# Performance work log

Measured on AMD Instinct MI355X. Metric: run time of the kernel, lower is better.

The kernel has to match this reference:

```python
import jax, jax.numpy as jnp
import numpy as np

N_NODES = 50000
N_EDGES = 800000
D = 128


def gcn_conv(x, W, b, src, dst, num_nodes):
    """PyG GCNConv: x @ W, add self-loops, symmetric normalization, scatter-add, + bias."""
    x = x @ W  # [N, out]
    loop = jnp.arange(num_nodes, dtype=src.dtype)
    s = jnp.concatenate([src, loop])  # [E+N]
    d = jnp.concatenate([dst, loop])
    w = jnp.ones(s.shape[0], x.dtype)  # edge_weight=None -> ones (self-loop fill=1)
    deg = jax.ops.segment_sum(w, d, num_segments=num_nodes)  # [N]
    dinv = jnp.where(deg > 0, jax.lax.rsqrt(deg), 0.0)
    norm = dinv[s] * dinv[d]  # [E+N]
    out = jax.ops.segment_sum(x[s] * norm[:, None], d, num_segments=num_nodes)
    return out + b


def setup_inputs() -> dict:
    key = jax.random.key(0)
    ks = jax.random.split(key, 8)
    sc = 1.0 / np.sqrt(D)
    x = jax.random.normal(ks[0], (N_NODES, D), dtype=jnp.float32)
    edge_index = jax.random.randint(ks[1], (2, N_EDGES), 0, N_NODES)
    W1 = jax.random.normal(ks[2], (D, D), dtype=jnp.float32) * sc
    W2 = jax.random.normal(ks[3], (D, D), dtype=jnp.float32) * sc
    W3 = jax.random.normal(ks[4], (D, D), dtype=jnp.float32) * sc
    b1 = jnp.zeros((D,), jnp.float32)
    b2 = jnp.zeros((D,), jnp.float32)
    b3 = jnp.zeros((D,), jnp.float32)
    return {"x": x, "edge_index": edge_index, "W1": W1, "b1": b1,
            "W2": W2, "b2": b2, "W3": W3, "b3": b3}


def reference(x, edge_index, W1, b1, W2, b2, W3, b3):
    src, dst = edge_index[0], edge_index[1]
    n = x.shape[0]
    x = jax.nn.relu(gcn_conv(x, W1, b1, src, dst, n))
    x = jax.nn.relu(gcn_conv(x, W2, b2, src, dst, n))
    return gcn_conv(x, W3, b3, src, dst, n)
```

## Files before the change

kernel.cpp:

```cpp
#include <hip/hip_runtime.h>
#include <hip/hip_fp16.h>
#include <math.h>

#define D 128
#define PADH 136

typedef __attribute__((ext_vector_type(8))) _Float16 half8;
typedef __attribute__((ext_vector_type(4))) float f32x4;


__global__ void prep_kernel(const float* __restrict__ W1, const float* __restrict__ W2,
                            const float* __restrict__ W3, __half* __restrict__ WhT,
                            int* __restrict__ cnt, int N) {
    int i = blockIdx.x * blockDim.x + threadIdx.x;
    if (i < 3 * D * D) {
        int l = i >> 14;
        int j = i & 16383;
        int n = j >> 7, k = j & 127;
        const float* W = (l == 0) ? W1 : (l == 1) ? W2 : W3;
        WhT[(size_t)i] = __float2half(W[(size_t)k * D + n]);
    }
    if (i < N) cnt[i] = 0;
}


__global__ void count_rank_kernel(const int* __restrict__ dst, int* __restrict__ cnt,
                                  int* __restrict__ rank, int E) {
    int e0 = (blockIdx.x * blockDim.x + threadIdx.x) * 8;
    if (e0 + 7 < E) {
        int4 da = *(const int4*)(dst + e0);
        int4 db = *(const int4*)(dst + e0 + 4);
        int4 ra, rb;
        ra.x = atomicAdd(&cnt[da.x], 1);
        ra.y = atomicAdd(&cnt[da.y], 1);
        ra.z = atomicAdd(&cnt[da.z], 1);
        ra.w = atomicAdd(&cnt[da.w], 1);
        rb.x = atomicAdd(&cnt[db.x], 1);
        rb.y = atomicAdd(&cnt[db.y], 1);
        rb.z = atomicAdd(&cnt[db.z], 1);
        rb.w = atomicAdd(&cnt[db.w], 1);
        *(int4*)(rank + e0)     = ra;
        *(int4*)(rank + e0 + 4) = rb;
    } else {
        for (int e = e0; e < E; ++e) rank[e] = atomicAdd(&cnt[dst[e]], 1);
    }
}

__global__ __launch_bounds__(1024) void scan_kernel(const int* __restrict__ cnt,
                                                    int* __restrict__ rowptr,
                                                    float* __restrict__ dinv,
                                                    int N) {
    __shared__ int wsum[16];
    int tid  = threadIdx.x;
    int lane = tid & 63;
    int wid  = tid >> 6;
    int C = ((N + 4095) / 4096) * 4;
    int start = tid * C;
    int end   = start + C; if (end > N) end = N;

    int local = 0;
    int i = start;
    for (; i + 3 < end; i += 4) {
        int4 v = *(const int4*)(cnt + i);
        local += v.x + v.y + v.z + v.w;
    }
    for (; i < end; ++i) local += cnt[i];

    int sc = local;
    #pragma unroll
    for (int off = 1; off < 64; off <<= 1) {
        int t = __shfl_up(sc, off, 64);
        if (lane >= off) sc += t;
    }
    if (lane == 63) wsum[wid] = sc;
    __syncthreads();
    if (tid < 16) {
        int w = wsum[tid];
        #pragma unroll
        for (int off = 1; off < 16; off <<= 1) {
            int t = __shfl_up(w, off, 16);
            if (tid >= off) w += t;
        }
        wsum[tid] = w;
    }
    __syncthreads();
    int run = ((wid > 0) ? wsum[wid - 1] : 0) + (sc - local);

    i = start;
    for (; i + 3 < end; i += 4) {
        int4 v = *(const int4*)(cnt + i);
        int4 rp;
        rp.x = run;
        rp.y = rp.x + v.x;
        rp.z = rp.y + v.y;
        rp.w = rp.z + v.z;
        run  = rp.w + v.w;
        *(int4*)(rowptr + i) = rp;
        float4 dv;
        dv.x = rsqrtf((float)v.x + 1.0f);
        dv.y = rsqrtf((float)v.y + 1.0f);
        dv.z = rsqrtf((float)v.z + 1.0f);
        dv.w = rsqrtf((float)v.w + 1.0f);
        *(float4*)(dinv + i) = dv;
    }
    for (; i < end; ++i) {
        int v = cnt[i];
        rowptr[i] = run; run += v;
        dinv[i] = rsqrtf((float)v + 1.0f);
    }
    if (tid == 0) rowptr[N] = wsum[15];
}


#define GATHER(vv, cc) __half2 vv = ((const __half2*)(g + (size_t)(cc) * D))[lane]

__device__ __forceinline__ float2 gather_row(const __half* __restrict__ g,
                                             const int* __restrict__ rowptr,
                                             const int* __restrict__ col,
                                             int row, int lane) {
    int s = rowptr[row], e = rowptr[row + 1];
    __half2 hself = ((const __half2*)(g + (size_t)row * D))[lane];
    float2 a0 = __half22float2(hself);
    float2 a1 = make_float2(0.f, 0.f), a2 = make_float2(0.f, 0.f),
           a3 = make_float2(0.f, 0.f), a4 = make_float2(0.f, 0.f),
           a5 = make_float2(0.f, 0.f), a6 = make_float2(0.f, 0.f),
           a7 = make_float2(0.f, 0.f);

    for (int base = s; base < e; base += 64) {
        int idx = base + lane;
        int myc = (idx < e) ? col[idx] : 0;
        int nb  = min(64, e - base);
        int j = 0;
        for (; j + 16 <= nb; j += 16) {
            int c0 = __shfl(myc, j + 0),  c1 = __shfl(myc, j + 1);
            int c2 = __shfl(myc, j + 2),  c3 = __shfl(myc, j + 3);
            int c4 = __shfl(myc, j + 4),  c5 = __shfl(myc, j + 5);
            int c6 = __shfl(myc, j + 6),  c7 = __shfl(myc, j + 7);
            int c8 = __shfl(myc, j + 8),  c9 = __shfl(myc, j + 9);
            int cA = __shfl(myc, j + 10), cB = __shfl(myc, j + 11);
            int cC = __shfl(myc, j + 12), cD = __shfl(myc, j + 13);
            int cE = __shfl(myc, j + 14), cF = __shfl(myc, j + 15);
            GATHER(v0, c0); GATHER(v1, c1); GATHER(v2, c2); GATHER(v3, c3);
            GATHER(v4, c4); GATHER(v5, c5); GATHER(v6, c6); GATHER(v7, c7);
            GATHER(v8, c8); GATHER(v9, c9); GATHER(vA, cA); GATHER(vB, cB);
            GATHER(vC, cC); GATHER(vD, cD); GATHER(vE, cE); GATHER(vF, cF);
            a0.x += __low2float(v0); a0.y += __high2float(v0);
            a1.x += __low2float(v1); a1.y += __high2float(v1);
            a2.x += __low2float(v2); a2.y += __high2float(v2);
            a3.x += __low2float(v3); a3.y += __high2float(v3);
            a4.x += __low2float(v4); a4.y += __high2float(v4);
            a5.x += __low2float(v5); a5.y += __high2float(v5);
            a6.x += __low2float(v6); a6.y += __high2float(v6);
            a7.x += __low2float(v7); a7.y += __high2float(v7);
            a0.x += __low2float(v8); a0.y += __high2float(v8);
            a1.x += __low2float(v9); a1.y += __high2float(v9);
            a2.x += __low2float(vA); a2.y += __high2float(vA);
            a3.x += __low2float(vB); a3.y += __high2float(vB);
            a4.x += __low2float(vC); a4.y += __high2float(vC);
            a5.x += __low2float(vD); a5.y += __high2float(vD);
            a6.x += __low2float(vE); a6.y += __high2float(vE);
            a7.x += __low2float(vF); a7.y += __high2float(vF);
        }
        for (; j + 8 <= nb; j += 8) {
            int c0 = __shfl(myc, j + 0), c1 = __shfl(myc, j + 1);
            int c2 = __shfl(myc, j + 2), c3 = __shfl(myc, j + 3);
            int c4 = __shfl(myc, j + 4), c5 = __shfl(myc, j + 5);
            int c6 = __shfl(myc, j + 6), c7 = __shfl(myc, j + 7);
            GATHER(v0, c0); GATHER(v1, c1); GATHER(v2, c2); GATHER(v3, c3);
            GATHER(v4, c4); GATHER(v5, c5); GATHER(v6, c6); GATHER(v7, c7);
            a0.x += __low2float(v0); a0.y += __high2float(v0);
            a1.x += __low2float(v1); a1.y += __high2float(v1);
            a2.x += __low2float(v2); a2.y += __high2float(v2);
            a3.x += __low2float(v3); a3.y += __high2float(v3);
            a4.x += __low2float(v4); a4.y += __high2float(v4);
            a5.x += __low2float(v5); a5.y += __high2float(v5);
            a6.x += __low2float(v6); a6.y += __high2float(v6);
            a7.x += __low2float(v7); a7.y += __high2float(v7);
        }
        for (; j + 4 <= nb; j += 4) {
            int c0 = __shfl(myc, j + 0), c1 = __shfl(myc, j + 1);
            int c2 = __shfl(myc, j + 2), c3 = __shfl(myc, j + 3);
            GATHER(v0, c0); GATHER(v1, c1); GATHER(v2, c2); GATHER(v3, c3);
            a0.x += __low2float(v0); a0.y += __high2float(v0);
            a1.x += __low2float(v1); a1.y += __high2float(v1);
            a2.x += __low2float(v2); a2.y += __high2float(v2);
            a3.x += __low2float(v3); a3.y += __high2float(v3);
        }
        for (; j < nb; ++j) {
            int c = __shfl(myc, j);
            GATHER(v, c);
            a0.x += __low2float(v); a0.y += __high2float(v);
        }
    }
    a0.x += a1.x + a2.x + a3.x + a4.x + a5.x + a6.x + a7.x;
    a0.y += a1.y + a2.y + a3.y + a4.y + a5.y + a6.y + a7.y;
    return a0;
}


__global__ __launch_bounds__(256) void fill_gemm1_kernel(
    const int* __restrict__ src, const int* __restrict__ dst,
    const int* __restrict__ rank, const int* __restrict__ rowptr,
    int* __restrict__ col, int E, int fill_blocks,
    const float* __restrict__ X, const __half* __restrict__ WhT,
    const float* __restrict__ dinv, __half* __restrict__ Y, int M) {
    int tid = threadIdx.x;
    if ((int)blockIdx.x < fill_blocks) {
        int e0 = (blockIdx.x * 256 + tid) * 8;
        if (e0 + 7 < E) {
            int4 da = *(const int4*)(dst + e0);
            int4 db = *(const int4*)(dst + e0 + 4);
            int4 ra = *(const int4*)(rank + e0);
            int4 rb = *(const int4*)(rank + e0 + 4);
            int4 sa = *(const int4*)(src + e0);
            int4 sb = *(const int4*)(src + e0 + 4);
            int p0 = rowptr[da.x] + ra.x;
            int p1 = rowptr[da.y] + ra.y;
            int p2 = rowptr[da.z] + ra.z;
            int p3 = rowptr[da.w] + ra.w;
            int p4 = rowptr[db.x] + rb.x;
            int p5 = rowptr[db.y] + rb.y;
            int p6 = rowptr[db.z] + rb.z;
            int p7 = rowptr[db.w] + rb.w;
            col[p0] = sa.x; col[p1] = sa.y; col[p2] = sa.z; col[p3] = sa.w;
            col[p4] = sb.x; col[p5] = sb.y; col[p6] = sb.z; col[p7] = sb.w;
        } else {
            for (int e = e0; e < E; ++e) col[rowptr[dst[e]] + rank[e]] = src[e];
        }
        return;
    }
    int bid  = blockIdx.x - fill_blocks;
    int wave = tid >> 6;
    int lane = tid & 63;
    int quad = lane >> 4;
    int l16  = lane & 15;
    int m0   = bid * 64 + wave * 16;
    if (m0 >= M) return;

    f32x4 acc[8];
    #pragma unroll
    for (int t = 0; t < 8; ++t) acc[t] = (f32x4)0.0f;

    const float* xrow = X + (size_t)(m0 + l16) * D;

    #pragma unroll
    for (int ks = 0; ks < 4; ++ks) {
        int k0 = ks * 32 + quad * 8;
        float4 x0 = *(const float4*)(xrow + k0);
        float4 x1 = *(const float4*)(xrow + k0 + 4);
        half8 a;
        a[0] = (_Float16)x0.x; a[1] = (_Float16)x0.y;
        a[2] = (_Float16)x0.z; a[3] = (_Float16)x0.w;
        a[4] = (_Float16)x1.x; a[5] = (_Float16)x1.y;
        a[6] = (_Float16)x1.z; a[7] = (_Float16)x1.w;
        #pragma unroll
        for (int t = 0; t < 8; ++t) {
            half8 b = *(const half8*)(WhT + (size_t)(t * 16 + l16) * D + k0);
            acc[t] = __builtin_amdgcn_mfma_f32_16x16x32_f16(a, b, acc[t], 0, 0, 0);
        }
    }

    float4 dv = *(const float4*)(dinv + m0 + quad * 4);
    float dvs[4] = {dv.x, dv.y, dv.z, dv.w};
    #pragma unroll
    for (int t = 0; t < 8; ++t) {
        #pragma unroll
        for (int r = 0; r < 4; ++r) {
            int grow = m0 + quad * 4 + r;
            Y[(size_t)grow * D + t * 16 + l16] = __float2half(acc[t][r] * dvs[r]);
        }
    }
}


__global__ __launch_bounds__(256) void agg_gemm_kernel(
    const __half* __restrict__ ysIn, const int* __restrict__ rowptr,
    const int* __restrict__ col, const float* __restrict__ dinv,
    const float* __restrict__ bias, const __half* __restrict__ WhT,
    __half* __restrict__ ysOut, int M) {
    __shared__ __half lds_h[16 * PADH];
    int tid  = threadIdx.x;
    int wave = tid >> 6;
    int lane = tid & 63;
    int rbase = blockIdx.x * 16;

    float2 bb = ((const float2*)bias)[lane];
    #pragma unroll
    for (int t = 0; t < 4; ++t) {
        int row = rbase + wave * 4 + t;
        if (row < M) {
            float2 a = gather_row(ysIn, rowptr, col, row, lane);
            float dv = dinv[row];
            float rx = bb.x + dv * a.x;
            float ry = bb.y + dv * a.y;
            __half2 hv = __floats2half2_rn(fmaxf(rx, 0.f), fmaxf(ry, 0.f));
            ((__half2*)(lds_h + (size_t)(wave * 4 + t) * PADH))[lane] = hv;
        }
    }
    __syncthreads();

    if (rbase >= M) return;
    int quad = lane >> 4;
    int l16  = lane & 15;
    int t0   = wave * 2;

    f32x4 acc0 = (f32x4)0.0f, acc1 = (f32x4)0.0f;
    const __half* arow = lds_h + (size_t)l16 * PADH;

    #pragma unroll
    for (int ks = 0; ks < 4; ++ks) {
        int k0 = ks * 32 + quad * 8;
        half8 a  = *(const half8*)(arow + k0);
        half8 b0 = *(const half8*)(WhT + (size_t)((t0 + 0) * 16 + l16) * D + k0);
        half8 b1 = *(const half8*)(WhT + (size_t)((t0 + 1) * 16 + l16) * D + k0);
        acc0 = __builtin_amdgcn_mfma_f32_16x16x32_f16(a, b0, acc0, 0, 0, 0);
        acc1 = __builtin_amdgcn_mfma_f32_16x16x32_f16(a, b1, acc1, 0, 0, 0);
    }

    #pragma unroll
    for (int r = 0; r < 4; ++r) {
        int grow = rbase + quad * 4 + r;
        if (grow < M) {
            float dvr = dinv[grow];
            ysOut[(size_t)grow * D + (t0 + 0) * 16 + l16] = __float2half(acc0[r] * dvr);
            ysOut[(size_t)grow * D + (t0 + 1) * 16 + l16] = __float2half(acc1[r] * dvr);
        }
    }
}


__global__ __launch_bounds__(256) void agg_final_kernel(
    const __half* __restrict__ ys, const int* __restrict__ rowptr,
    const int* __restrict__ col, const float* __restrict__ dinv,
    const float* __restrict__ b, float* __restrict__ out, int N) {
    int gwave = (blockIdx.x * blockDim.x + threadIdx.x) >> 6;
    int lane  = threadIdx.x & 63;
    if (gwave >= N) return;
    float2 a  = gather_row(ys, rowptr, col, gwave, lane);
    float dv  = dinv[gwave];
    float2 bb = ((const float2*)b)[lane];
    ((float2*)(out + (size_t)gwave * D))[lane] = make_float2(bb.x + dv * a.x, bb.y + dv * a.y);
}


extern "C" void kernel_launch(void* const* d_in, const int* in_sizes, int n_in,
                              void* d_out, int out_size, void* d_ws, size_t ws_size,
                              hipStream_t stream) {
    const float* x   = (const float*)d_in[0];
    const int*   ei  = (const int*)d_in[1];
    const float* W1  = (const float*)d_in[2];
    const float* b1  = (const float*)d_in[3];
    const float* W2  = (const float*)d_in[4];
    const float* b2  = (const float*)d_in[5];
    const float* W3  = (const float*)d_in[6];
    const float* b3  = (const float*)d_in[7];
    float* out = (float*)d_out;

    const int N = in_sizes[0] / D;
    const int E = in_sizes[1] / 2;
    const int* src = ei;
    const int* dst = ei + E;

    char* ws = (char*)d_ws;
    size_t off = 0;
    auto alloc = [&](size_t bytes) {
        void* p = ws + off;
        off = (off + bytes + 255) & ~(size_t)255;
        return p;
    };
    __half* ys    = (__half*)alloc((size_t)N * D * sizeof(__half));
    __half* hs    = (__half*)alloc((size_t)N * D * sizeof(__half));
    int*   cnt    = (int*)alloc((size_t)N * sizeof(int));
    int*   rowptr = (int*)alloc((size_t)(N + 1) * sizeof(int));
    float* dinv   = (float*)alloc((size_t)N * sizeof(float));
    int*   rank   = (int*)alloc((size_t)E * sizeof(int));
    int*   col    = (int*)alloc((size_t)E * sizeof(int));
    __half* WhT   = (__half*)alloc((size_t)3 * D * D * sizeof(__half));
    (void)ws_size; (void)n_in; (void)out_size;

    int prep_threads = (3 * D * D > N) ? 3 * D * D : N;
    prep_kernel<<<(prep_threads + 255) / 256, 256, 0, stream>>>(W1, W2, W3, WhT, cnt, N);

    const int egrid = ((E + 7) / 8 + 255) / 256;
    count_rank_kernel<<<egrid, 256, 0, stream>>>(dst, cnt, rank, E);
    scan_kernel<<<1, 1024, 0, stream>>>(cnt, rowptr, dinv, N);

    const int gemm1_grid = (N + 63) / 64;
    fill_gemm1_kernel<<<egrid + gemm1_grid, 256, 0, stream>>>(
        src, dst, rank, rowptr, col, E, egrid, x, WhT, dinv, ys, N);

    const int agg_gemm_grid = (N + 15) / 16;
    agg_gemm_kernel<<<agg_gemm_grid, 256, 0, stream>>>(ys, rowptr, col, dinv, b1, WhT + 16384, hs, N);
    agg_gemm_kernel<<<agg_gemm_grid, 256, 0, stream>>>(hs, rowptr, col, dinv, b2, WhT + 32768, ys, N);

    const int agg_grid = (N * 64 + 255) / 256;
    agg_final_kernel<<<agg_grid, 256, 0, stream>>>(ys, rowptr, col, dinv, b3, out, N);
}
```

Measured before the change: 311.4 us.

## Gather four rows per wave with 16-byte loads; shard CSR fill by destination range

The aggregation gather now assigns 16 lanes per destination row, so one wave handles four rows at once and each lane loads eight halves with a 16-byte load instead of a half2. This raises bytes per load instruction and keeps more independent rows in flight for the roughly 16-neighbour average degree. The CSR column fill is split into eight destination-range shards, each rescanning all edges but writing only its own range, to localize scattered writes at the cost of reading dst eight times. The final aggregation kernel launches a quarter as many waves.

```diff
diff --git a/kernel.cpp b/kernel.cpp
--- a/kernel.cpp
+++ b/kernel.cpp
@@ -14,9 +14,7 @@
                             int* __restrict__ cnt, int N) {
     int i = blockIdx.x * blockDim.x + threadIdx.x;
     if (i < 3 * D * D) {
-        int l = i >> 14;
-        int j = i & 16383;
-        int n = j >> 7, k = j & 127;
+        int l = i >> 14, j = i & 16383, n = j >> 7, k = j & 127;
         const float* W = (l == 0) ? W1 : (l == 1) ? W2 : W3;
         WhT[(size_t)i] = __float2half(W[(size_t)k * D + n]);
     }
@@ -90,11 +88,8 @@
     for (; i + 3 < end; i += 4) {
         int4 v = *(const int4*)(cnt + i);
         int4 rp;
-        rp.x = run;
-        rp.y = rp.x + v.x;
-        rp.z = rp.y + v.y;
-        rp.w = rp.z + v.z;
-        run  = rp.w + v.w;
+        rp.x = run; rp.y = rp.x + v.x; rp.z = rp.y + v.y; rp.w = rp.z + v.z;
+        run = rp.w + v.w;
         *(int4*)(rowptr + i) = rp;
         float4 dv;
         dv.x = rsqrtf((float)v.x + 1.0f);
@@ -112,120 +107,127 @@
 }
 
 
-#define GATHER(vv, cc) __half2 vv = ((const __half2*)(g + (size_t)(cc) * D))[lane]
-
-__device__ __forceinline__ float2 gather_row(const __half* __restrict__ g,
-                                             const int* __restrict__ rowptr,
-                                             const int* __restrict__ col,
-                                             int row, int lane) {
+__device__ __forceinline__ void gather4(const __half* __restrict__ g,
+                                        const int* __restrict__ rowptr,
+                                        const int* __restrict__ col,
+                                        int row, int lane, float* __restrict__ acc) {
+    int grp = lane >> 4;
+    int l16 = lane & 15;
+    int gb  = grp << 4;
     int s = rowptr[row], e = rowptr[row + 1];
-    __half2 hself = ((const __half2*)(g + (size_t)row * D))[lane];
-    float2 a0 = __half22float2(hself);
-    float2 a1 = make_float2(0.f, 0.f), a2 = make_float2(0.f, 0.f),
-           a3 = make_float2(0.f, 0.f), a4 = make_float2(0.f, 0.f),
-           a5 = make_float2(0.f, 0.f), a6 = make_float2(0.f, 0.f),
-           a7 = make_float2(0.f, 0.f);
-
-    for (int base = s; base < e; base += 64) {
-        int idx = base + lane;
+
+    half8 hs = ((const half8*)(g + (size_t)row * D))[l16];
+    float a0 = (float)hs[0], a1 = (float)hs[1], a2 = (float)hs[2], a3 = (float)hs[3];
+    float a4 = (float)hs[4], a5 = (float)hs[5], a6 = (float)hs[6], a7 = (float)hs[7];
+    float b0 = 0.f, b1 = 0.f, b2 = 0.f, b3 = 0.f, b4 = 0.f, b5 = 0.f, b6 = 0.f, b7 = 0.f;
+
+    for (int base = s; base < e; base += 16) {
+        int idx = base + l16;
         int myc = (idx < e) ? col[idx] : 0;
-        int nb  = min(64, e - base);
+        int nb  = min(16, e - base);
         int j = 0;
-        for (; j + 16 <= nb; j += 16) {
-            int c0 = __shfl(myc, j + 0),  c1 = __shfl(myc, j + 1);
-            int c2 = __shfl(myc, j + 2),  c3 = __shfl(myc, j + 3);
-            int c4 = __shfl(myc, j + 4),  c5 = __shfl(myc, j + 5);
-            int c6 = __shfl(myc, j + 6),  c7 = __shfl(myc, j + 7);
-            int c8 = __shfl(myc, j + 8),  c9 = __shfl(myc, j + 9);
-            int cA = __shfl(myc, j + 10), cB = __shfl(myc, j + 11);
-            int cC = __shfl(myc, j + 12), cD = __shfl(myc, j + 13);
-            int cE = __shfl(myc, j + 14), cF = __shfl(myc, j + 15);
-            GATHER(v0, c0); GATHER(v1, c1); GATHER(v2, c2); GATHER(v3, c3);
-            GATHER(v4, c4); GATHER(v5, c5); GATHER(v6, c6); GATHER(v7, c7);
-            GATHER(v8, c8); GATHER(v9, c9); GATHER(vA, cA); GATHER(vB, cB);
-            GATHER(vC, cC); GATHER(vD, cD); GATHER(vE, cE); GATHER(vF, cF);
-            a0.x += __low2float(v0); a0.y += __high2float(v0);
-            a1.x += __low2float(v1); a1.y += __high2float(v1);
-            a2.x += __low2float(v2); a2.y += __high2float(v2);
-            a3.x += __low2float(v3); a3.y += __high2float(v3);
-            a4.x += __low2float(v4); a4.y += __high2float(v4);
-            a5.x += __low2float(v5); a5.y += __high2float(v5);
-            a6.x += __low2float(v6); a6.y += __high2float(v6);
-            a7.x += __low2float(v7); a7.y += __high2float(v7);
-            a0.x += __low2float(v8); a0.y += __high2float(v8);
-            a1.x += __low2float(v9); a1.y += __high2float(v9);
-            a2.x += __low2float(vA); a2.y += __high2float(vA);
-            a3.x += __low2float(vB); a3.y += __high2float(vB);
-            a4.x += __low2float(vC); a4.y += __high2float(vC);
-            a5.x += __low2float(vD); a5.y += __high2float(vD);
-            a6.x += __low2float(vE); a6.y += __high2float(vE);
-            a7.x += __low2float(vF); a7.y += __high2float(vF);
-        }
         for (; j + 8 <= nb; j += 8) {
-            int c0 = __shfl(myc, j + 0), c1 = __shfl(myc, j + 1);
-            int c2 = __shfl(myc, j + 2), c3 = __shfl(myc, j + 3);
-            int c4 = __shfl(myc, j + 4), c5 = __shfl(myc, j + 5);
-            int c6 = __shfl(myc, j + 6), c7 = __shfl(myc, j + 7);
-            GATHER(v0, c0); GATHER(v1, c1); GATHER(v2, c2); GATHER(v3, c3);
-            GATHER(v4, c4); GATHER(v5, c5); GATHER(v6, c6); GATHER(v7, c7);
-            a0.x += __low2float(v0); a0.y += __high2float(v0);
-            a1.x += __low2float(v1); a1.y += __high2float(v1);
-            a2.x += __low2float(v2); a2.y += __high2float(v2);
-            a3.x += __low2float(v3); a3.y += __high2float(v3);
-            a4.x += __low2float(v4); a4.y += __high2float(v4);
-            a5.x += __low2float(v5); a5.y += __high2float(v5);
-            a6.x += __low2float(v6); a6.y += __high2float(v6);
-            a7.x += __low2float(v7); a7.y += __high2float(v7);
+            int c0 = __shfl(myc, gb + j + 0), c1 = __shfl(myc, gb + j + 1);
+            int c2 = __shfl(myc, gb + j + 2), c3 = __shfl(myc, gb + j + 3);
+            int c4 = __shfl(myc, gb + j + 4), c5 = __shfl(myc, gb + j + 5);
+            int c6 = __shfl(myc, gb + j + 6), c7 = __shfl(myc, gb + j + 7);
+            half8 v0 = ((const half8*)(g + (size_t)c0 * D))[l16];
+            half8 v1 = ((const half8*)(g + (size_t)c1 * D))[l16];
+            half8 v2 = ((const half8*)(g + (size_t)c2 * D))[l16];
+            half8 v3 = ((const half8*)(g + (size_t)c3 * D))[l16];
+            half8 v4 = ((const half8*)(g + (size_t)c4 * D))[l16];
+            half8 v5 = ((const half8*)(g + (size_t)c5 * D))[l16];
+            half8 v6 = ((const half8*)(g + (size_t)c6 * D))[l16];
+            half8 v7 = ((const half8*)(g + (size_t)c7 * D))[l16];
+            a0 += (float)v0[0]; a1 += (float)v0[1]; a2 += (float)v0[2]; a3 += (float)v0[3];
+            a4 += (float)v0[4]; a5 += (float)v0[5]; a6 += (float)v0[6]; a7 += (float)v0[7];
+            b0 += (float)v1[0]; b1 += (float)v1[1]; b2 += (float)v1[2]; b3 += (float)v1[3];
+            b4 += (float)v1[4]; b5 += (float)v1[5]; b6 += (float)v1[6]; b7 += (float)v1[7];
+            a0 += (float)v2[0]; a1 += (float)v2[1]; a2 += (float)v2[2]; a3 += (float)v2[3];
+            a4 += (float)v2[4]; a5 += (float)v2[5]; a6 += (float)v2[6]; a7 += (float)v2[7];
+            b0 += (float)v3[0]; b1 += (float)v3[1]; b2 += (float)v3[2]; b3 += (float)v3[3];
+            b4 += (float)v3[4]; b5 += (float)v3[5]; b6 += (float)v3[6]; b7 += (float)v3[7];
+            a0 += (float)v4[0]; a1 += (float)v4[1]; a2 += (float)v4[2]; a3 += (float)v4[3];
+            a4 += (float)v4[4]; a5 += (float)v4[5]; a6 += (float)v4[6]; a7 += (float)v4[7];
+            b0 += (float)v5[0]; b1 += (float)v5[1]; b2 += (float)v5[2]; b3 += (float)v5[3];
+            b4 += (float)v5[4]; b5 += (float)v5[5]; b6 += (float)v5[6]; b7 += (float)v5[7];
+            a0 += (float)v6[0]; a1 += (float)v6[1]; a2 += (float)v6[2]; a3 += (float)v6[3];
+            a4 += (float)v6[4]; a5 += (float)v6[5]; a6 += (float)v6[6]; a7 += (float)v6[7];
+            b0 += (float)v7[0]; b1 += (float)v7[1]; b2 += (float)v7[2]; b3 += (float)v7[3];
+            b4 += (float)v7[4]; b5 += (float)v7[5]; b6 += (float)v7[6]; b7 += (float)v7[7];
         }
         for (; j + 4 <= nb; j += 4) {
-            int c0 = __shfl(myc, j + 0), c1 = __shfl(myc, j + 1);
-            int c2 = __shfl(myc, j + 2), c3 = __shfl(myc, j + 3);
-            GATHER(v0, c0); GATHER(v1, c1); GATHER(v2, c2); GATHER(v3, c3);
-            a0.x += __low2float(v0); a0.y += __high2float(v0);
-            a1.x += __low2float(v1); a1.y += __high2float(v1);
-            a2.x += __low2float(v2); a2.y += __high2float(v2);
-            a3.x += __low2float(v3); a3.y += __high2float(v3);
+            int c0 = __shfl(myc, gb + j + 0), c1 = __shfl(myc, gb + j + 1);
+            int c2 = __shfl(myc, gb + j + 2), c3 = __shfl(myc, gb + j + 3);
+            half8 v0 = ((const half8*)(g + (size_t)c0 * D))[l16];
+            half8 v1 = ((const half8*)(g + (size_t)c1 * D))[l16];
+            half8 v2 = ((const half8*)(g + (size_t)c2 * D))[l16];
+            half8 v3 = ((const half8*)(g + (size_t)c3 * D))[l16];
+            a0 += (float)v0[0]; a1 += (float)v0[1]; a2 += (float)v0[2]; a3 += (float)v0[3];
+            a4 += (float)v0[4]; a5 += (float)v0[5]; a6 += (float)v0[6]; a7 += (float)v0[7];
+            b0 += (float)v1[0]; b1 += (float)v1[1]; b2 += (float)v1[2]; b3 += (float)v1[3];
+            b4 += (float)v1[4]; b5 += (float)v1[5]; b6 += (float)v1[6]; b7 += (float)v1[7];
+            a0 += (float)v2[0]; a1 += (float)v2[1]; a2 += (float)v2[2]; a3 += (float)v2[3];
+            a4 += (float)v2[4]; a5 += (float)v2[5]; a6 += (float)v2[6]; a7 += (float)v2[7];
+            b0 += (float)v3[0]; b1 += (float)v3[1]; b2 += (float)v3[2]; b3 += (float)v3[3];
+            b4 += (float)v3[4]; b5 += (float)v3[5]; b6 += (float)v3[6]; b7 += (float)v3[7];
         }
         for (; j < nb; ++j) {
-            int c = __shfl(myc, j);
-            GATHER(v, c);
-            a0.x += __low2float(v); a0.y += __high2float(v);
-        }
-    }
-    a0.x += a1.x + a2.x + a3.x + a4.x + a5.x + a6.x + a7.x;
-    a0.y += a1.y + a2.y + a3.y + a4.y + a5.y + a6.y + a7.y;
-    return a0;
+            int c = __shfl(myc, gb + j);
+            half8 v = ((const half8*)(g + (size_t)c * D))[l16];
+            a0 += (float)v[0]; a1 += (float)v[1]; a2 += (float)v[2]; a3 += (float)v[3];
+            a4 += (float)v[4]; a5 += (float)v[5]; a6 += (float)v[6]; a7 += (float)v[7];
+        }
+    }
+    acc[0] = a0 + b0; acc[1] = a1 + b1; acc[2] = a2 + b2; acc[3] = a3 + b3;
+    acc[4] = a4 + b4; acc[5] = a5 + b5; acc[6] = a6 + b6; acc[7] = a7 + b7;
 }
 
 
 __global__ __launch_bounds__(256) void fill_gemm1_kernel(
     const int* __restrict__ src, const int* __restrict__ dst,
     const int* __restrict__ rank, const int* __restrict__ rowptr,
-    int* __restrict__ col, int E, int fill_blocks,
+    int* __restrict__ col, int E, int fill_blocks, int N,
     const float* __restrict__ X, const __half* __restrict__ WhT,
     const float* __restrict__ dinv, __half* __restrict__ Y, int M) {
     int tid = threadIdx.x;
     if ((int)blockIdx.x < fill_blocks) {
-        int e0 = (blockIdx.x * 256 + tid) * 8;
-        if (e0 + 7 < E) {
-            int4 da = *(const int4*)(dst + e0);
-            int4 db = *(const int4*)(dst + e0 + 4);
-            int4 ra = *(const int4*)(rank + e0);
-            int4 rb = *(const int4*)(rank + e0 + 4);
-            int4 sa = *(const int4*)(src + e0);
-            int4 sb = *(const int4*)(src + e0 + 4);
-            int p0 = rowptr[da.x] + ra.x;
-            int p1 = rowptr[da.y] + ra.y;
-            int p2 = rowptr[da.z] + ra.z;
-            int p3 = rowptr[da.w] + ra.w;
-            int p4 = rowptr[db.x] + rb.x;
-            int p5 = rowptr[db.y] + rb.y;
-            int p6 = rowptr[db.z] + rb.z;
-            int p7 = rowptr[db.w] + rb.w;
-            col[p0] = sa.x; col[p1] = sa.y; col[p2] = sa.z; col[p3] = sa.w;
-            col[p4] = sb.x; col[p5] = sb.y; col[p6] = sb.z; col[p7] = sb.w;
-        } else {
-            for (int e = e0; e < E; ++e) col[rowptr[dst[e]] + rank[e]] = src[e];
+        int shard = blockIdx.x & 7;
+        int sub   = blockIdx.x >> 3;
+        int nsub  = fill_blocks >> 3;
+        int chunk = (N + 7) >> 3;
+        int lo = shard * chunk;
+        unsigned span = (unsigned)(min(lo + chunk, N) - lo);
+        const int NO = (E + 7) / 8;
+        for (int c = sub * 256 + tid; c < NO; c += nsub * 256) {
+            int e0 = c * 8;
+            if (e0 + 7 < E) {
+                int4 da = *(const int4*)(dst + e0);
+                int4 db = *(const int4*)(dst + e0 + 4);
+                bool i0 = (unsigned)(da.x - lo) < span, i1 = (unsigned)(da.y - lo) < span;
+                bool i2 = (unsigned)(da.z - lo) < span, i3 = (unsigned)(da.w - lo) < span;
+                bool i4 = (unsigned)(db.x - lo) < span, i5 = (unsigned)(db.y - lo) < span;
+                bool i6 = (unsigned)(db.z - lo) < span, i7 = (unsigned)(db.w - lo) < span;
+                if (i0 | i1 | i2 | i3 | i4 | i5 | i6 | i7) {
+                    int4 ra = *(const int4*)(rank + e0);
+                    int4 rb = *(const int4*)(rank + e0 + 4);
+                    int4 sa = *(const int4*)(src + e0);
+                    int4 sb = *(const int4*)(src + e0 + 4);
+                    if (i0) col[rowptr[da.x] + ra.x] = sa.x;
+                    if (i1) col[rowptr[da.y] + ra.y] = sa.y;
+                    if (i2) col[rowptr[da.z] + ra.z] = sa.z;
+                    if (i3) col[rowptr[da.w] + ra.w] = sa.w;
+                    if (i4) col[rowptr[db.x] + rb.x] = sb.x;
+                    if (i5) col[rowptr[db.y] + rb.y] = sb.y;
+                    if (i6) col[rowptr[db.z] + rb.z] = sb.z;
+                    if (i7) col[rowptr[db.w] + rb.w] = sb.w;
+                }
+            } else {
+                for (int e = e0; e < E; ++e) {
+                    int d = dst[e];
+                    if ((unsigned)(d - lo) < span) col[rowptr[d] + rank[e]] = src[e];
+                }
+            }
         }
         return;
     }
@@ -240,9 +242,7 @@
     f32x4 acc[8];
     #pragma unroll
     for (int t = 0; t < 8; ++t) acc[t] = (f32x4)0.0f;
-
     const float* xrow = X + (size_t)(m0 + l16) * D;
-
     #pragma unroll
     for (int ks = 0; ks < 4; ++ks) {
         int k0 = ks * 32 + quad * 8;
@@ -259,7 +259,6 @@
             acc[t] = __builtin_amdgcn_mfma_f32_16x16x32_f16(a, b, acc[t], 0, 0, 0);
         }
     }
-
     float4 dv = *(const float4*)(dinv + m0 + quad * 4);
     float dvs[4] = {dv.x, dv.y, dv.z, dv.w};
     #pragma unroll
@@ -282,31 +281,34 @@
     int tid  = threadIdx.x;
     int wave = tid >> 6;
     int lane = tid & 63;
+    int grp  = lane >> 4;
+    int l16  = lane & 15;
     int rbase = blockIdx.x * 16;
-
-    float2 bb = ((const float2*)bias)[lane];
-    #pragma unroll
-    for (int t = 0; t < 4; ++t) {
-        int row = rbase + wave * 4 + t;
-        if (row < M) {
-            float2 a = gather_row(ysIn, rowptr, col, row, lane);
-            float dv = dinv[row];
-            float rx = bb.x + dv * a.x;
-            float ry = bb.y + dv * a.y;
-            __half2 hv = __floats2half2_rn(fmaxf(rx, 0.f), fmaxf(ry, 0.f));
-            ((__half2*)(lds_h + (size_t)(wave * 4 + t) * PADH))[lane] = hv;
-        }
-    }
+    int lrow  = wave * 4 + grp;
+    int row   = min(rbase + lrow, M - 1);
+
+    float acc8[8];
+    gather4(ysIn, rowptr, col, row, lane, acc8);
+
+    float dv = dinv[row];
+    float4 bb0 = ((const float4*)bias)[l16 * 2];
+    float4 bb1 = ((const float4*)bias)[l16 * 2 + 1];
+    half8 hv;
+    hv[0] = (_Float16)fmaxf(bb0.x + dv * acc8[0], 0.f);
+    hv[1] = (_Float16)fmaxf(bb0.y + dv * acc8[1], 0.f);
+    hv[2] = (_Float16)fmaxf(bb0.z + dv * acc8[2], 0.f);
+    hv[3] = (_Float16)fmaxf(bb0.w + dv * acc8[3], 0.f);
+    hv[4] = (_Float16)fmaxf(bb1.x + dv * acc8[4], 0.f);
+    hv[5] = (_Float16)fmaxf(bb1.y + dv * acc8[5], 0.f);
+    hv[6] = (_Float16)fmaxf(bb1.z + dv * acc8[6], 0.f);
+    hv[7] = (_Float16)fmaxf(bb1.w + dv * acc8[7], 0.f);
+    ((half8*)(lds_h + (size_t)lrow * PADH))[l16] = hv;
     __syncthreads();
 
-    if (rbase >= M) return;
     int quad = lane >> 4;
-    int l16  = lane & 15;
     int t0   = wave * 2;
-
     f32x4 acc0 = (f32x4)0.0f, acc1 = (f32x4)0.0f;
     const __half* arow = lds_h + (size_t)l16 * PADH;
-
     #pragma unroll
     for (int ks = 0; ks < 4; ++ks) {
         int k0 = ks * 32 + quad * 8;
@@ -316,7 +318,6 @@
         acc0 = __builtin_amdgcn_mfma_f32_16x16x32_f16(a, b0, acc0, 0, 0, 0);
         acc1 = __builtin_amdgcn_mfma_f32_16x16x32_f16(a, b1, acc1, 0, 0, 0);
     }
-
     #pragma unroll
     for (int r = 0; r < 4; ++r) {
         int grow = rbase + quad * 4 + r;
@@ -335,11 +336,32 @@
     const float* __restrict__ b, float* __restrict__ out, int N) {
     int gwave = (blockIdx.x * blockDim.x + threadIdx.x) >> 6;
     int lane  = threadIdx.x & 63;
-    if (gwave >= N) return;
-    float2 a  = gather_row(ys, rowptr, col, gwave, lane);
-    float dv  = dinv[gwave];
-    float2 bb = ((const float2*)b)[lane];
-    ((float2*)(out + (size_t)gwave * D))[lane] = make_float2(bb.x + dv * a.x, bb.y + dv * a.y);
+    int grp   = lane >> 4;
+    int l16   = lane & 15;
+    int rbase = gwave * 4;
+    if (rbase >= N) return;
+    int row = min(rbase + grp, N - 1);
+
+    float acc8[8];
+    gather4(ys, rowptr, col, row, lane, acc8);
+
+    if (rbase + grp < N) {
+        float dv = dinv[row];
+        float4 bb0 = ((const float4*)b)[l16 * 2];
+        float4 bb1 = ((const float4*)b)[l16 * 2 + 1];
+        float4 r0, r1;
+        r0.x = bb0.x + dv * acc8[0];
+        r0.y = bb0.y + dv * acc8[1];
+        r0.z = bb0.z + dv * acc8[2];
+        r0.w = bb0.w + dv * acc8[3];
+        r1.x = bb1.x + dv * acc8[4];
+        r1.y = bb1.y + dv * acc8[5];
+        r1.z = bb1.z + dv * acc8[6];
+        r1.w = bb1.w + dv * acc8[7];
+        float* op = out + (size_t)row * D + l16 * 8;
+        ((float4*)op)[0] = r0;
+        ((float4*)op)[1] = r1;
+    }
 }
 
 
@@ -381,18 +403,20 @@
     int prep_threads = (3 * D * D > N) ? 3 * D * D : N;
     prep_kernel<<<(prep_threads + 255) / 256, 256, 0, stream>>>(W1, W2, W3, WhT, cnt, N);
 
-    const int egrid = ((E + 7) / 8 + 255) / 256;
+    const int NO = (E + 7) / 8;
+    const int egrid = (NO + 255) / 256;
     count_rank_kernel<<<egrid, 256, 0, stream>>>(dst, cnt, rank, E);
     scan_kernel<<<1, 1024, 0, stream>>>(cnt, rowptr, dinv, N);
 
+    const int FB = ((egrid + 7) / 8) * 8;
     const int gemm1_grid = (N + 63) / 64;
-    fill_gemm1_kernel<<<egrid + gemm1_grid, 256, 0, stream>>>(
-        src, dst, rank, rowptr, col, E, egrid, x, WhT, dinv, ys, N);
+    fill_gemm1_kernel<<<FB + gemm1_grid, 256, 0, stream>>>(
+        src, dst, rank, rowptr, col, E, FB, N, x, WhT, dinv, ys, N);
 
     const int agg_gemm_grid = (N + 15) / 16;
     agg_gemm_kernel<<<agg_gemm_grid, 256, 0, stream>>>(ys, rowptr, col, dinv, b1, WhT + 16384, hs, N);
     agg_gemm_kernel<<<agg_gemm_grid, 256, 0, stream>>>(hs, rowptr, col, dinv, b2, WhT + 32768, ys, N);
 
-    const int agg_grid = (N * 64 + 255) / 256;
-    agg_final_kernel<<<agg_grid, 256, 0, stream>>>(ys, rowptr, col, dinv, b3, out, N);
-}
+    const int aggf_grid = (((N + 3) / 4) * 64 + 255) / 256;
+    agg_final_kernel<<<aggf_grid, 256, 0, stream>>>(ys, rowptr, col, dinv, b3, out, N);
+}
```

Result: faster. 298.0 us (-4.3%).
